# Optimization experiments

Hardware: AMD Instinct MI355X
Metric: run time of the kernel (lower is better)

## Reference

```python
import jax, jax.numpy as jnp
import numpy as np

B = 4096
D = 1024
WEIGHT = 1.0
EPS = 1e-7  # Keras K.epsilon()


def setup_inputs() -> dict:
    key = jax.random.key(0)
    k1, k2 = jax.random.split(key)
    return {
        "left": jax.random.normal(k1, (B, D), dtype=jnp.float32),
        "right": jax.random.normal(k2, (B, D), dtype=jnp.float32),
        "temperature": jnp.zeros((1,), dtype=jnp.float32),
    }


def _l2_normalize(x):
    # matches l2_norm: sqrt(max(sum(x^2), eps))
    sq = jnp.sum(jnp.square(x), axis=-1, keepdims=True)
    return x / jnp.sqrt(jnp.maximum(sq, EPS))


def reference(left, right, temperature):
    ln = _l2_normalize(left)   # [B, D]
    rn = _l2_normalize(right)  # [B, D]
    scale = jnp.exp(temperature)  # (1,) broadcasts
    logits_left = jnp.einsum("bd,cd->bc", ln, rn) * scale   # [B, B]
    logits_right = logits_left.T                             # rn @ ln.T * scale
    prob_left = jax.nn.softmax(logits_left, axis=-1)
    prob_right = jax.nn.softmax(logits_right, axis=-1)
    # NOTE: the original calls CCE(prob, labels), i.e. y_true=prob, y_pred=eye.
    # Keras clips y_pred to [eps, 1-eps]; loss = -sum(y_true * log(clip(y_pred))).
    labels = jnp.eye(B, dtype=jnp.float32)
    log_clipped = jnp.log(jnp.clip(labels, EPS, 1.0 - EPS))  # diag: log(1-eps), off: log(eps)
    loss_left = -jnp.sum(prob_left * log_clipped)
    loss_right = -jnp.sum(prob_right * log_clipped)
    loss = (loss_left + loss_right) / 2.0 / B
    return WEIGHT * loss
```

## Files before the change

kernel.cpp:

```cpp
#include <hip/hip_runtime.h>
#include <hip/hip_bf16.h>

#define Bn 4096
#define Dk 1024
#define EPSF 1e-7f

typedef float f32x16 __attribute__((ext_vector_type(16)));
typedef int i32x4 __attribute__((ext_vector_type(4)));
typedef int i32x8 __attribute__((ext_vector_type(8)));

__device__ __forceinline__ void async_copy16(const void* g, void* l) {
    __builtin_amdgcn_global_load_lds((__attribute__((address_space(1))) void*)(uintptr_t)g,
                                     (__attribute__((address_space(3))) void*)l, 16, 0, 0);
}

__global__ __launch_bounds__(256)
void nrm_kernel(const float4* __restrict__ left, const float4* __restrict__ right,
                unsigned char* __restrict__ lnb8, unsigned char* __restrict__ rnb8,
                float* __restrict__ diag, float* __restrict__ rowsum,
                float* __restrict__ colsum)
{
    const int row = blockIdx.x;
    const int t = threadIdx.x;
    const int idx = row * (Dk / 4) + t;
    const float4 l = left[idx];
    const float4 r = right[idx];
    float sl = l.x * l.x + l.y * l.y + l.z * l.z + l.w * l.w;
    float sr = r.x * r.x + r.y * r.y + r.z * r.z + r.w * r.w;
    float slr = l.x * r.x + l.y * r.y + l.z * r.z + l.w * r.w;
    #pragma unroll
    for (int off = 1; off < 64; off <<= 1) {
        sl += __shfl_xor(sl, off);
        sr += __shfl_xor(sr, off);
        slr += __shfl_xor(slr, off);
    }
    __shared__ float red[3][4];
    const int wave = t >> 6, lane = t & 63;
    if (lane == 0) { red[0][wave] = sl; red[1][wave] = sr; red[2][wave] = slr; }
    __syncthreads();
    sl = red[0][0] + red[0][1] + red[0][2] + red[0][3];
    sr = red[1][0] + red[1][1] + red[1][2] + red[1][3];
    const float invl = 1.0f / sqrtf(fmaxf(sl, EPSF));
    const float invr = 1.0f / sqrtf(fmaxf(sr, EPSF));
    const float sL = 8.0f * invl;
    const float sR = 8.0f * invr;
    int pkL = __builtin_amdgcn_cvt_pk_fp8_f32(l.x * sL, l.y * sL, 0, false);
    pkL = __builtin_amdgcn_cvt_pk_fp8_f32(l.z * sL, l.w * sL, pkL, true);
    int pkR = __builtin_amdgcn_cvt_pk_fp8_f32(r.x * sR, r.y * sR, 0, false);
    pkR = __builtin_amdgcn_cvt_pk_fp8_f32(r.z * sR, r.w * sR, pkR, true);
    const int dst = row * Dk + 4 * t;
    *(unsigned*)(lnb8 + dst) = (unsigned)pkL;
    *(unsigned*)(rnb8 + dst) = (unsigned)pkR;
    if (t == 0) {
        const float d = red[2][0] + red[2][1] + red[2][2] + red[2][3];
        diag[row] = d * invl * invr;
        rowsum[row] = 0.f;
        colsum[row] = 0.f;
    }
}

__global__ __launch_bounds__(256, 1)
void gemm_sm_kernel(const unsigned char* __restrict__ lnb8,
                    const unsigned char* __restrict__ rnb8,
                    const float* __restrict__ temp,
                    float* __restrict__ rowsum, float* __restrict__ colsum)
{
    __shared__ __align__(16) unsigned char As[2][256 * 64];
    __shared__ __align__(16) unsigned char Bs[2][256 * 64];

    const int tid = threadIdx.x;
    const int wave = tid >> 6;
    const int lane = tid & 63;
    const int bm0 = blockIdx.y * 256;
    const int bn0 = blockIdx.x * 256;

    const int srow = lane >> 2;
    const int sj = lane & 3;
    int goffA[4], lofsA[4];
    #pragma unroll
    for (int i = 0; i < 4; ++i) {
        const int rloc = wave * 64 + i * 16 + srow;
        goffA[i] = rloc * Dk + 16 * (sj ^ ((rloc >> 1) & 3));
        lofsA[i] = (wave * 64 + i * 16) * 64;
    }
    int goffB[4], lofsB[4];
    #pragma unroll
    for (int i = 0; i < 4; ++i) {
        const int rloc = wave * 64 + i * 16 + srow;
        goffB[i] = rloc * Dk + 16 * (sj ^ ((rloc >> 1) & 3));
        lofsB[i] = (wave * 64 + i * 16) * 64;
    }
    const unsigned char* baseA = lnb8 + (size_t)bm0 * Dk;
    const unsigned char* baseB = rnb8 + (size_t)bn0 * Dk;

    const int wm = (wave & 1) * 128;
    const int wn = (wave >> 1) * 128;
    const int r32 = lane & 31;
    const int h = lane >> 5;
    int aoff[4][2], boff[4][2];
    #pragma unroll
    for (int mi = 0; mi < 4; ++mi) {
        const int row = wm + mi * 32 + r32;
        const int key = (row >> 1) & 3;
        aoff[mi][0] = row * 64 + 16 * ((2 * h) ^ key);
        aoff[mi][1] = row * 64 + 16 * ((2 * h + 1) ^ key);
    }
    #pragma unroll
    for (int ni = 0; ni < 4; ++ni) {
        const int row = wn + ni * 32 + r32;
        const int key = (row >> 1) & 3;
        boff[ni][0] = row * 64 + 16 * ((2 * h) ^ key);
        boff[ni][1] = row * 64 + 16 * ((2 * h + 1) ^ key);
    }

    f32x16 acc[4][4];
    #pragma unroll
    for (int mi = 0; mi < 4; ++mi)
        #pragma unroll
        for (int ni = 0; ni < 4; ++ni)
            #pragma unroll
            for (int r = 0; r < 16; ++r)
                acc[mi][ni][r] = 0.f;

    #pragma unroll
    for (int i = 0; i < 4; ++i) async_copy16(baseA + goffA[i], &As[0][lofsA[i]]);
    #pragma unroll
    for (int i = 0; i < 4; ++i) async_copy16(baseB + goffB[i], &Bs[0][lofsB[i]]);

    #pragma unroll 2
    for (int it = 0; it < 16; ++it) {
        const int cur = it & 1;
        const int nxt = cur ^ 1;
        const int knext = ((it + 1) & 15) * 64;
        #pragma unroll
        for (int i = 0; i < 4; ++i) async_copy16(baseA + goffA[i] + knext, &As[nxt][lofsA[i]]);
        #pragma unroll
        for (int i = 0; i < 4; ++i) async_copy16(baseB + goffB[i] + knext, &Bs[nxt][lofsB[i]]);
        asm volatile("s_waitcnt vmcnt(8)\n\ts_barrier" ::: "memory");
        i32x8 af[4], bf[4];
        #pragma unroll
        for (int mi = 0; mi < 4; ++mi) {
            const i32x4 lo = *(const i32x4*)(&As[cur][aoff[mi][0]]);
            const i32x4 hi = *(const i32x4*)(&As[cur][aoff[mi][1]]);
            af[mi] = __builtin_shufflevector(lo, hi, 0, 1, 2, 3, 4, 5, 6, 7);
        }
        #pragma unroll
        for (int ni = 0; ni < 4; ++ni) {
            const i32x4 lo = *(const i32x4*)(&Bs[cur][boff[ni][0]]);
            const i32x4 hi = *(const i32x4*)(&Bs[cur][boff[ni][1]]);
            bf[ni] = __builtin_shufflevector(lo, hi, 0, 1, 2, 3, 4, 5, 6, 7);
        }
        #pragma unroll
        for (int mi = 0; mi < 4; ++mi)
            #pragma unroll
            for (int ni = 0; ni < 4; ++ni)
                acc[mi][ni] = __builtin_amdgcn_mfma_scale_f32_32x32x64_f8f6f4(
                    af[mi], bf[ni], acc[mi][ni],
                    0, 0,
                    0, 0x7f7f7f7f,
                    0, 0x7f7f7f7f);
        asm volatile("s_barrier" ::: "memory");
    }

    const float scale = __expf(temp[0]);
    const float dq = 0.015625f * scale;
    #pragma unroll
    for (int mi = 0; mi < 4; ++mi)
        #pragma unroll
        for (int ni = 0; ni < 4; ++ni)
            #pragma unroll
            for (int r = 0; r < 16; ++r)
                acc[mi][ni][r] = __expf(dq * acc[mi][ni][r] - scale);

    #pragma unroll
    for (int mi = 0; mi < 4; ++mi) {
        #pragma unroll
        for (int r = 0; r < 16; ++r) {
            float v = acc[mi][0][r] + acc[mi][1][r] + acc[mi][2][r] + acc[mi][3][r];
            v += __shfl_xor(v, 1);
            v += __shfl_xor(v, 2);
            v += __shfl_xor(v, 4);
            v += __shfl_xor(v, 8);
            v += __shfl_xor(v, 16);
            if (r32 == 0)
                atomicAdd(&rowsum[bm0 + wm + mi * 32 + (r & 3) + 8 * (r >> 2) + 4 * h], v);
        }
    }
    #pragma unroll
    for (int ni = 0; ni < 4; ++ni) {
        float v = 0.f;
        #pragma unroll
        for (int mi = 0; mi < 4; ++mi)
            #pragma unroll
            for (int r = 0; r < 16; ++r)
                v += acc[mi][ni][r];
        v += __shfl_xor(v, 32);
        if (h == 0)
            atomicAdd(&colsum[bn0 + wn + ni * 32 + r32], v);
    }
}

__global__ __launch_bounds__(256)
void loss_kernel(const float* __restrict__ diag, const float* __restrict__ rowsum,
                 const float* __restrict__ colsum, const float* __restrict__ temp,
                 float* __restrict__ out)
{
    const int t = threadIdx.x;
    const float scale = __expf(temp[0]);
    float dL = 0.f, dR = 0.f;
    for (int i = t; i < Bn; i += 256) {
        const float e = __expf(scale * (diag[i] - 1.0f));
        dL += e * __builtin_amdgcn_rcpf(rowsum[i]);
        dR += e * __builtin_amdgcn_rcpf(colsum[i]);
    }
    #pragma unroll
    for (int off = 1; off < 64; off <<= 1) {
        dL += __shfl_xor(dL, off);
        dR += __shfl_xor(dR, off);
    }
    __shared__ float rd[2][4];
    const int wave = t >> 6, lane = t & 63;
    if (lane == 0) { rd[0][wave] = dL; rd[1][wave] = dR; }
    __syncthreads();
    if (t == 0) {
        dL = rd[0][0] + rd[0][1] + rd[0][2] + rd[0][3];
        dR = rd[1][0] + rd[1][1] + rd[1][2] + rd[1][3];
        const float logeps = logf(EPSF);
        const float log1m = logf(1.0f - EPSF);
        const float lossL = -(dL * log1m + ((float)Bn - dL) * logeps);
        const float lossR = -(dR * log1m + ((float)Bn - dR) * logeps);
        out[0] = (lossL + lossR) * 0.5f / (float)Bn;
    }
}

extern "C" void kernel_launch(void* const* d_in, const int* in_sizes, int n_in,
                              void* d_out, int out_size, void* d_ws, size_t ws_size,
                              hipStream_t stream) {
    (void)in_sizes; (void)n_in; (void)out_size; (void)ws_size;
    const float* left = (const float*)d_in[0];
    const float* right = (const float*)d_in[1];
    const float* temp = (const float*)d_in[2];

    char* ws = (char*)d_ws;
    unsigned char* lnb8 = (unsigned char*)ws;
    unsigned char* rnb8 = (unsigned char*)(ws + (size_t)Bn * Dk);
    float* diag = (float*)(ws + 2 * (size_t)Bn * Dk);
    float* rowsum = diag + Bn;
    float* colsum = rowsum + Bn;

    nrm_kernel<<<Bn, 256, 0, stream>>>((const float4*)left, (const float4*)right,
                                       lnb8, rnb8, diag, rowsum, colsum);
    dim3 g2(Bn / 256, Bn / 256);
    gemm_sm_kernel<<<g2, 256, 0, stream>>>(lnb8, rnb8, temp, rowsum, colsum);
    loss_kernel<<<1, 256, 0, stream>>>(diag, rowsum, colsum, temp, (float*)d_out);
}
```

Before: 131.2 us.

## Use 8-wave blocks with triple-buffered LDS and interleaved MFMA/prefetch schedule

The GEMM+softmax-sum kernel moves from 4 waves with double buffering to 8 waves (512 threads, up to 2 blocks/CU) with a three-stage LDS ring, prefetching two K-steps ahead. Each wave now computes a 128x64 sub-tile, halving accumulator registers. The inner loop is split into four phases that interleave LDS fragment loads, single async global->LDS copies and MFMA pairs, using s_setprio and sched_barrier to encourage overlap. The intent is to hide load latency and raise occupancy, at the cost of many more barriers per iteration and 96KB of LDS per block, which may limit co-residency.

```diff
diff --git a/kernel.cpp b/kernel.cpp
--- a/kernel.cpp
+++ b/kernel.cpp
@@ -4,6 +4,7 @@
 #define Bn 4096
 #define Dk 1024
 #define EPSF 1e-7f
+#define ATILE (256 * 64)
 
 typedef float f32x16 __attribute__((ext_vector_type(16)));
 typedef int i32x4 __attribute__((ext_vector_type(4)));
@@ -59,14 +60,14 @@
     }
 }
 
-__global__ __launch_bounds__(256, 1)
+__global__ __launch_bounds__(512, 2)
 void gemm_sm_kernel(const unsigned char* __restrict__ lnb8,
                     const unsigned char* __restrict__ rnb8,
                     const float* __restrict__ temp,
                     float* __restrict__ rowsum, float* __restrict__ colsum)
 {
-    __shared__ __align__(16) unsigned char As[2][256 * 64];
-    __shared__ __align__(16) unsigned char Bs[2][256 * 64];
+    __shared__ __align__(16) unsigned char Ash[3 * ATILE];
+    __shared__ __align__(16) unsigned char Bsh[3 * ATILE];
 
     const int tid = threadIdx.x;
     const int wave = tid >> 6;
@@ -76,28 +77,21 @@
 
     const int srow = lane >> 2;
     const int sj = lane & 3;
-    int goffA[4], lofsA[4];
-    #pragma unroll
-    for (int i = 0; i < 4; ++i) {
-        const int rloc = wave * 64 + i * 16 + srow;
+    int goffA[2], lofsA[2];
+    #pragma unroll
+    for (int i = 0; i < 2; ++i) {
+        const int rloc = wave * 32 + i * 16 + srow;
         goffA[i] = rloc * Dk + 16 * (sj ^ ((rloc >> 1) & 3));
-        lofsA[i] = (wave * 64 + i * 16) * 64;
-    }
-    int goffB[4], lofsB[4];
-    #pragma unroll
-    for (int i = 0; i < 4; ++i) {
-        const int rloc = wave * 64 + i * 16 + srow;
-        goffB[i] = rloc * Dk + 16 * (sj ^ ((rloc >> 1) & 3));
-        lofsB[i] = (wave * 64 + i * 16) * 64;
+        lofsA[i] = (wave * 32 + i * 16) * 64;
     }
     const unsigned char* baseA = lnb8 + (size_t)bm0 * Dk;
     const unsigned char* baseB = rnb8 + (size_t)bn0 * Dk;
 
     const int wm = (wave & 1) * 128;
-    const int wn = (wave >> 1) * 128;
+    const int wn = (wave >> 1) * 64;
     const int r32 = lane & 31;
     const int h = lane >> 5;
-    int aoff[4][2], boff[4][2];
+    int aoff[4][2], boff[2][2];
     #pragma unroll
     for (int mi = 0; mi < 4; ++mi) {
         const int row = wm + mi * 32 + r32;
@@ -106,60 +100,119 @@
         aoff[mi][1] = row * 64 + 16 * ((2 * h + 1) ^ key);
     }
     #pragma unroll
-    for (int ni = 0; ni < 4; ++ni) {
+    for (int ni = 0; ni < 2; ++ni) {
         const int row = wn + ni * 32 + r32;
         const int key = (row >> 1) & 3;
         boff[ni][0] = row * 64 + 16 * ((2 * h) ^ key);
         boff[ni][1] = row * 64 + 16 * ((2 * h + 1) ^ key);
     }
 
-    f32x16 acc[4][4];
+    f32x16 acc[4][2];
     #pragma unroll
     for (int mi = 0; mi < 4; ++mi)
         #pragma unroll
-        for (int ni = 0; ni < 4; ++ni)
+        for (int ni = 0; ni < 2; ++ni)
             #pragma unroll
             for (int r = 0; r < 16; ++r)
                 acc[mi][ni][r] = 0.f;
 
     #pragma unroll
-    for (int i = 0; i < 4; ++i) async_copy16(baseA + goffA[i], &As[0][lofsA[i]]);
-    #pragma unroll
-    for (int i = 0; i < 4; ++i) async_copy16(baseB + goffB[i], &Bs[0][lofsB[i]]);
-
-    #pragma unroll 2
-    for (int it = 0; it < 16; ++it) {
-        const int cur = it & 1;
-        const int nxt = cur ^ 1;
-        const int knext = ((it + 1) & 15) * 64;
-        #pragma unroll
-        for (int i = 0; i < 4; ++i) async_copy16(baseA + goffA[i] + knext, &As[nxt][lofsA[i]]);
-        #pragma unroll
-        for (int i = 0; i < 4; ++i) async_copy16(baseB + goffB[i] + knext, &Bs[nxt][lofsB[i]]);
-        asm volatile("s_waitcnt vmcnt(8)\n\ts_barrier" ::: "memory");
-        i32x8 af[4], bf[4];
-        #pragma unroll
-        for (int mi = 0; mi < 4; ++mi) {
-            const i32x4 lo = *(const i32x4*)(&As[cur][aoff[mi][0]]);
-            const i32x4 hi = *(const i32x4*)(&As[cur][aoff[mi][1]]);
-            af[mi] = __builtin_shufflevector(lo, hi, 0, 1, 2, 3, 4, 5, 6, 7);
-        }
-        #pragma unroll
-        for (int ni = 0; ni < 4; ++ni) {
-            const i32x4 lo = *(const i32x4*)(&Bs[cur][boff[ni][0]]);
-            const i32x4 hi = *(const i32x4*)(&Bs[cur][boff[ni][1]]);
-            bf[ni] = __builtin_shufflevector(lo, hi, 0, 1, 2, 3, 4, 5, 6, 7);
-        }
-        #pragma unroll
-        for (int mi = 0; mi < 4; ++mi)
-            #pragma unroll
-            for (int ni = 0; ni < 4; ++ni)
-                acc[mi][ni] = __builtin_amdgcn_mfma_scale_f32_32x32x64_f8f6f4(
-                    af[mi], bf[ni], acc[mi][ni],
-                    0, 0,
-                    0, 0x7f7f7f7f,
-                    0, 0x7f7f7f7f);
-        asm volatile("s_barrier" ::: "memory");
+    for (int b = 0; b < 2; ++b) {
+        #pragma unroll
+        for (int i = 0; i < 2; ++i)
+            async_copy16(baseA + goffA[i] + b * 64, &Ash[b * ATILE + lofsA[i]]);
+        #pragma unroll
+        for (int i = 0; i < 2; ++i)
+            async_copy16(baseB + goffA[i] + b * 64, &Bsh[b * ATILE + lofsA[i]]);
+    }
+
+    int cur = 0;
+    #pragma unroll 1
+    for (int t = 0; t < 16; ++t) {
+        const int nb = (cur >= 1) ? (cur - 1) : 2;
+        if (t == 15) asm volatile("s_waitcnt vmcnt(0)" ::: "memory");
+        else         asm volatile("s_waitcnt vmcnt(4)" ::: "memory");
+        __builtin_amdgcn_s_barrier();
+
+        const unsigned char* At = &Ash[cur * ATILE];
+        const unsigned char* Bt = &Bsh[cur * ATILE];
+        unsigned char* An = &Ash[nb * ATILE];
+        unsigned char* Bns = &Bsh[nb * ATILE];
+        const int kn = (t + 2) * 64;
+        const bool pf = (t < 14);
+
+        i32x8 af0, af1, af2, af3, bf0, bf1;
+        {
+            const i32x4 alo = *(const i32x4*)(At + aoff[0][0]);
+            const i32x4 ahi = *(const i32x4*)(At + aoff[0][1]);
+            af0 = __builtin_shufflevector(alo, ahi, 0, 1, 2, 3, 4, 5, 6, 7);
+            const i32x4 b0l = *(const i32x4*)(Bt + boff[0][0]);
+            const i32x4 b0h = *(const i32x4*)(Bt + boff[0][1]);
+            bf0 = __builtin_shufflevector(b0l, b0h, 0, 1, 2, 3, 4, 5, 6, 7);
+            const i32x4 b1l = *(const i32x4*)(Bt + boff[1][0]);
+            const i32x4 b1h = *(const i32x4*)(Bt + boff[1][1]);
+            bf1 = __builtin_shufflevector(b1l, b1h, 0, 1, 2, 3, 4, 5, 6, 7);
+            if (pf) async_copy16(baseA + goffA[0] + kn, An + lofsA[0]);
+        }
+        __builtin_amdgcn_s_barrier();
+        asm volatile("s_waitcnt lgkmcnt(0)" ::: "memory");
+        __builtin_amdgcn_sched_barrier(0);
+        __builtin_amdgcn_s_setprio(1);
+        acc[0][0] = __builtin_amdgcn_mfma_scale_f32_32x32x64_f8f6f4(
+            af0, bf0, acc[0][0], 0, 0, 0, 0x7f7f7f7f, 0, 0x7f7f7f7f);
+        acc[0][1] = __builtin_amdgcn_mfma_scale_f32_32x32x64_f8f6f4(
+            af0, bf1, acc[0][1], 0, 0, 0, 0x7f7f7f7f, 0, 0x7f7f7f7f);
+        __builtin_amdgcn_s_setprio(0);
+
+        {
+            const i32x4 alo = *(const i32x4*)(At + aoff[1][0]);
+            const i32x4 ahi = *(const i32x4*)(At + aoff[1][1]);
+            af1 = __builtin_shufflevector(alo, ahi, 0, 1, 2, 3, 4, 5, 6, 7);
+            if (pf) async_copy16(baseA + goffA[1] + kn, An + lofsA[1]);
+        }
+        __builtin_amdgcn_s_barrier();
+        asm volatile("s_waitcnt lgkmcnt(0)" ::: "memory");
+        __builtin_amdgcn_sched_barrier(0);
+        __builtin_amdgcn_s_setprio(1);
+        acc[1][0] = __builtin_amdgcn_mfma_scale_f32_32x32x64_f8f6f4(
+            af1, bf0, acc[1][0], 0, 0, 0, 0x7f7f7f7f, 0, 0x7f7f7f7f);
+        acc[1][1] = __builtin_amdgcn_mfma_scale_f32_32x32x64_f8f6f4(
+            af1, bf1, acc[1][1], 0, 0, 0, 0x7f7f7f7f, 0, 0x7f7f7f7f);
+        __builtin_amdgcn_s_setprio(0);
+
+        {
+            const i32x4 alo = *(const i32x4*)(At + aoff[2][0]);
+            const i32x4 ahi = *(const i32x4*)(At + aoff[2][1]);
+            af2 = __builtin_shufflevector(alo, ahi, 0, 1, 2, 3, 4, 5, 6, 7);
+            if (pf) async_copy16(baseB + goffA[0] + kn, Bns + lofsA[0]);
+        }
+        __builtin_amdgcn_s_barrier();
+        asm volatile("s_waitcnt lgkmcnt(0)" ::: "memory");
+        __builtin_amdgcn_sched_barrier(0);
+        __builtin_amdgcn_s_setprio(1);
+        acc[2][0] = __builtin_amdgcn_mfma_scale_f32_32x32x64_f8f6f4(
+            af2, bf0, acc[2][0], 0, 0, 0, 0x7f7f7f7f, 0, 0x7f7f7f7f);
+        acc[2][1] = __builtin_amdgcn_mfma_scale_f32_32x32x64_f8f6f4(
+            af2, bf1, acc[2][1], 0, 0, 0, 0x7f7f7f7f, 0, 0x7f7f7f7f);
+        __builtin_amdgcn_s_setprio(0);
+
+        {
+            const i32x4 alo = *(const i32x4*)(At + aoff[3][0]);
+            const i32x4 ahi = *(const i32x4*)(At + aoff[3][1]);
+            af3 = __builtin_shufflevector(alo, ahi, 0, 1, 2, 3, 4, 5, 6, 7);
+            if (pf) async_copy16(baseB + goffA[1] + kn, Bns + lofsA[1]);
+        }
+        __builtin_amdgcn_s_barrier();
+        asm volatile("s_waitcnt lgkmcnt(0)" ::: "memory");
+        __builtin_amdgcn_sched_barrier(0);
+        __builtin_amdgcn_s_setprio(1);
+        acc[3][0] = __builtin_amdgcn_mfma_scale_f32_32x32x64_f8f6f4(
+            af3, bf0, acc[3][0], 0, 0, 0, 0x7f7f7f7f, 0, 0x7f7f7f7f);
+        acc[3][1] = __builtin_amdgcn_mfma_scale_f32_32x32x64_f8f6f4(
+            af3, bf1, acc[3][1], 0, 0, 0, 0x7f7f7f7f, 0, 0x7f7f7f7f);
+        __builtin_amdgcn_s_setprio(0);
+
+        cur = (cur == 2) ? 0 : cur + 1;
     }
 
     const float scale = __expf(temp[0]);
@@ -167,7 +220,7 @@
     #pragma unroll
     for (int mi = 0; mi < 4; ++mi)
         #pragma unroll
-        for (int ni = 0; ni < 4; ++ni)
+        for (int ni = 0; ni < 2; ++ni)
             #pragma unroll
             for (int r = 0; r < 16; ++r)
                 acc[mi][ni][r] = __expf(dq * acc[mi][ni][r] - scale);
@@ -176,7 +229,7 @@
     for (int mi = 0; mi < 4; ++mi) {
         #pragma unroll
         for (int r = 0; r < 16; ++r) {
-            float v = acc[mi][0][r] + acc[mi][1][r] + acc[mi][2][r] + acc[mi][3][r];
+            float v = acc[mi][0][r] + acc[mi][1][r];
             v += __shfl_xor(v, 1);
             v += __shfl_xor(v, 2);
             v += __shfl_xor(v, 4);
@@ -187,7 +240,7 @@
         }
     }
     #pragma unroll
-    for (int ni = 0; ni < 4; ++ni) {
+    for (int ni = 0; ni < 2; ++ni) {
         float v = 0.f;
         #pragma unroll
         for (int mi = 0; mi < 4; ++mi)
@@ -251,6 +304,6 @@
     nrm_kernel<<<Bn, 256, 0, stream>>>((const float4*)left, (const float4*)right,
                                        lnb8, rnb8, diag, rowsum, colsum);
     dim3 g2(Bn / 256, Bn / 256);
-    gemm_sm_kernel<<<g2, 256, 0, stream>>>(lnb8, rnb8, temp, rowsum, colsum);
+    gemm_sm_kernel<<<g2, 512, 0, stream>>>(lnb8, rnb8, temp, rowsum, colsum);
     loss_kernel<<<1, 256, 0, stream>>>(diag, rowsum, colsum, temp, (float*)d_out);
 }
```

Result: no change. 130.1 us (-0.9%).
